# Performance work log

Measured on AMD Instinct MI355X. Metric: run time of the kernel, lower is better.

## Reference

```python
import jax, jax.numpy as jnp
import numpy as np

DIM = 1024
NUM_HEADS = 16
HEAD_DIM = DIM // NUM_HEADS
SCALE = HEAD_DIM ** -0.5
B, LQ, LK = 2, 2048, 2048


def setup_inputs() -> dict:
    key = jax.random.key(0)
    ks = jax.random.split(key, 12)
    init = 1.0 / np.sqrt(DIM)  # ~ torch Linear default scale
    inp = {
        "q": jax.random.normal(ks[0], (B, LQ, DIM), jnp.float32),
        "k": jax.random.normal(ks[1], (B, LK, DIM), jnp.float32),
        "v": jax.random.normal(ks[2], (B, LK, DIM), jnp.float32),
        "kv_mask": jnp.ones((B, LK), jnp.int32),
        "Wq": jax.random.uniform(ks[3], (DIM, DIM), jnp.float32, -init, init),
        "bq": jax.random.uniform(ks[4], (DIM,), jnp.float32, -init, init),
        "Wk": jax.random.uniform(ks[5], (DIM, DIM), jnp.float32, -init, init),
        "bk": jax.random.uniform(ks[6], (DIM,), jnp.float32, -init, init),
        "Wv": jax.random.uniform(ks[7], (DIM, DIM), jnp.float32, -init, init),
        "bv": jax.random.uniform(ks[8], (DIM,), jnp.float32, -init, init),
        "Wo": jax.random.uniform(ks[9], (DIM, DIM), jnp.float32, -init, init),
        "bo": jax.random.uniform(ks[10], (DIM,), jnp.float32, -init, init),
    }
    return inp


def reference(q, k, v, kv_mask, Wq, bq, Wk, bk, Wv, bv, Wo, bo):
    Bq, Lq, D = q.shape
    Lk = k.shape[1]
    H, Hd = NUM_HEADS, HEAD_DIM
    # projections (torch Linear: x @ W.T + b); split heads -> [B, H, L, Hd]
    qh = (q @ Wq.T + bq).reshape(Bq, Lq, H, Hd).transpose(0, 2, 1, 3)
    kh = (k @ Wk.T + bk).reshape(Bq, Lk, H, Hd).transpose(0, 2, 1, 3)
    vh = (v @ Wv.T + bv).reshape(Bq, Lk, H, Hd).transpose(0, 2, 1, 3)
    # scores [B, H, Lq, Lk]
    attn = jnp.einsum("bhqd,bhkd->bhqk", qh, kh) * SCALE
    mask = (kv_mask != 0)[:, None, None, :]
    attn = jnp.where(mask, attn, -jnp.inf)
    attn = jax.nn.softmax(attn, axis=-1)
    # dropout is identity at inference (p applied only in train mode)
    out = jnp.einsum("bhqk,bhkd->bhqd", attn, vh)
    out = out.transpose(0, 2, 1, 3).reshape(Bq, Lq, D)
    return out @ Wo.T + bo
```

## Files before the change

### kernel.cpp

```cpp
#include <hip/hip_runtime.h>
#include <stdint.h>

typedef unsigned short u16;
typedef __attribute__((ext_vector_type(8))) __bf16 bf16x8;
typedef __attribute__((ext_vector_type(4))) float f32x4;
typedef __attribute__((ext_vector_type(2))) unsigned int uint32x2;

#define DIM 1024
#define NH 16
#define HD 64
#define BSZ 2
#define LQ 2048
#define LK 2048
#define SCALE_LOG2E 0.18033688011112043f
#define MNEG -3.0e38f


static __device__ __forceinline__ float b2f(u16 u) {
  union { uint32_t i; float f; } v; v.i = ((uint32_t)u) << 16; return v.f;
}
static __device__ __forceinline__ u16 f2b(float f) {
  uint32_t x = __float_as_uint(f);
  return (u16)((x + 0x7fffu + ((x >> 16) & 1u)) >> 16);
}
static __device__ __forceinline__ uint32_t pk2r(float lo, float hi) {
  uint32_t a = __float_as_uint(lo) + 0x8000u;
  uint32_t b = __float_as_uint(hi) + 0x8000u;
  return __builtin_amdgcn_perm(b, a, 0x07060302u);
}
static __device__ __forceinline__ uint32_t cvtpk(float lo, float hi) {
  uint32_t r;
  asm("v_cvt_pk_bf16_f32 %0, %1, %2" : "=v"(r) : "v"(lo), "v"(hi));
  return r;
}
static __device__ __forceinline__ f32x4 zero4() {
  f32x4 z; z[0] = 0.f; z[1] = 0.f; z[2] = 0.f; z[3] = 0.f; return z;
}
static __device__ __forceinline__ float exp2c(float s) {
  float r;
  asm("v_exp_f32 %0, %1\n\ts_nop 0" : "=v"(r) : "v"(fminf(s, 30.0f)));
  return r;
}
static __device__ __forceinline__ void gload_lds16(const u16* g, u16* l) {
  __builtin_amdgcn_global_load_lds(
      (const __attribute__((address_space(1))) void*)g,
      (__attribute__((address_space(3))) void*)l, 16, 0, 0);
}

__global__ void mask_allvalid(const int* __restrict__ kvmask, int* allv) {
  int b = blockIdx.x;
  int base = b * LK + threadIdx.x * 8;
  int ok = 1;
#pragma unroll
  for (int j = 0; j < 8; ++j) ok &= (kvmask[base + j] != 0);
  unsigned long long m = __ballot(ok != 0);
  if ((threadIdx.x & 63) == 0 && m != ~0ULL) atomicAnd(&allv[b], 0);
}

struct ConvArgs {
  const float* src[11];
  long long cum[12];
  u16* dst;
};

__global__ void convert_inputs(ConvArgs ca) {
  long long c = (long long)blockIdx.x * blockDim.x + threadIdx.x;
  long long e0 = c * 8;
  if (e0 >= ca.cum[11]) return;
  int s = 0;
  while (e0 >= ca.cum[s + 1]) ++s;
  const float* sp = ca.src[s] + (e0 - ca.cum[s]);
  union { uint4 v; uint32_t w[4]; } t;
#pragma unroll
  for (int j = 0; j < 4; ++j) t.w[j] = pk2r(sp[2 * j], sp[2 * j + 1]);
  *(uint4*)(ca.dst + e0) = t.v;
}

struct GemmArgs {
  const u16* X[3];
  const u16* W[3];
  const u16* Bias[3];
  void* Y[3];
  float osc[3];
  int f32out;
  int vtz;
};

__global__ __launch_bounds__(256, 3) void gemm_bt_bias(GemmArgs ga) {
  const int K = DIM, N = DIM;
  __shared__ u16 smem[17408];
  u16* const Al = smem;
  u16* const Bl = smem + 8192;
  const int tid = threadIdx.x;
  const int wave = tid >> 6, lane = tid & 63;
  const int wm = wave >> 1, wn = wave & 1;
  const int lrow = lane & 15, quad = lane >> 4;
  const int z = blockIdx.z;
  const u16* X = ga.X[z];
  const u16* W = ga.W[z];
  const u16* Bias = ga.Bias[z];
  const float osc = ga.osc[z];
  const int m0 = blockIdx.x * 128;
  const int n0 = blockIdx.y * 128;

  f32x4 acc[4][4];
#pragma unroll
  for (int i = 0; i < 4; ++i)
#pragma unroll
    for (int j = 0; j < 4; ++j) acc[i][j] = zero4();

  const int cbase = wave * 256;
  for (int k0 = 0; k0 < K; k0 += 64) {
    __syncthreads();
#pragma unroll
    for (int i = 0; i < 4; ++i) {
      int c = cbase + i * 64 + lane;
      int row = c >> 3, colb = c & 7;
      gload_lds16(X + (size_t)(m0 + row) * K + k0 + colb * 8,
                  &Al[(cbase + i * 64) * 8]);
      gload_lds16(W + (size_t)(n0 + row) * K + k0 + colb * 8,
                  &Bl[(cbase + i * 64) * 8]);
    }
    __syncthreads();
#pragma unroll
    for (int ks = 0; ks < 2; ++ks) {
      bf16x8 af[4], bfr[4];
#pragma unroll
      for (int t = 0; t < 4; ++t)
        af[t] = *(const bf16x8*)&Al[(wm * 64 + t * 16 + lrow) * 64 + ks * 32 + quad * 8];
#pragma unroll
      for (int t = 0; t < 4; ++t)
        bfr[t] = *(const bf16x8*)&Bl[(wn * 64 + t * 16 + lrow) * 64 + ks * 32 + quad * 8];
#pragma unroll
      for (int mt = 0; mt < 4; ++mt)
#pragma unroll
        for (int nt = 0; nt < 4; ++nt)
          acc[mt][nt] = __builtin_amdgcn_mfma_f32_16x16x32_bf16(af[mt], bfr[nt], acc[mt][nt], 0, 0, 0);
    }
  }

  if (z == ga.vtz) {
    u16* Yv = (u16*)ga.Y[z];
    u16* const VT = smem;
    __syncthreads();
#pragma unroll
    for (int nt = 0; nt < 4; ++nt) {
      int colL = wn * 64 + nt * 16 + lrow;
      float bv = b2f(Bias[n0 + colL]);
#pragma unroll
      for (int mt = 0; mt < 4; ++mt) {
        int keyL = wm * 64 + mt * 16 + quad * 4;
        uint2 w;
        w.x = pk2r((acc[mt][nt][0] + bv) * osc, (acc[mt][nt][1] + bv) * osc);
        w.y = pk2r((acc[mt][nt][2] + bv) * osc, (acc[mt][nt][3] + bv) * osc);
        *(uint2*)&VT[colL * 136 + keyL] = w;
      }
    }
    __syncthreads();
    const int bb = m0 >> 11, key0 = m0 & 2047;
#pragma unroll
    for (int i = 0; i < 8; ++i) {
      int c = i * 256 + tid;
      int colL = c >> 4, k8 = c & 15;
      int hh = (n0 + colL) >> 6, dd = (n0 + colL) & 63;
      *(uint4*)(Yv + ((size_t)(bb * NH + hh) * HD + dd) * LK + key0 + k8 * 8) =
          *(const uint4*)&VT[colL * 136 + k8 * 8];
    }
  } else if (ga.f32out) {
    float* Yf = (float*)ga.Y[z];
#pragma unroll
    for (int nt = 0; nt < 4; ++nt) {
      int col = n0 + wn * 64 + nt * 16 + lrow;
      float bv = b2f(Bias[col]);
#pragma unroll
      for (int mt = 0; mt < 4; ++mt) {
        int rowb = m0 + wm * 64 + mt * 16 + quad * 4;
#pragma unroll
        for (int r = 0; r < 4; ++r)
          Yf[(size_t)(rowb + r) * N + col] = (acc[mt][nt][r] + bv) * osc;
      }
    }
  } else {
    u16* Yv = (u16*)ga.Y[z];
#pragma unroll
    for (int nt = 0; nt < 4; ++nt) {
      int col = n0 + wn * 64 + nt * 16 + lrow;
      float bv = b2f(Bias[col]);
#pragma unroll
      for (int mt = 0; mt < 4; ++mt) {
        int rowb = m0 + wm * 64 + mt * 16 + quad * 4;
#pragma unroll
        for (int r = 0; r < 4; ++r)
          Yv[(size_t)(rowb + r) * N + col] = f2b((acc[mt][nt][r] + bv) * osc);
      }
    }
  }
}

__global__ __launch_bounds__(256, 3) void attn_fused(
    const u16* __restrict__ qp, const u16* __restrict__ kp,
    const u16* __restrict__ vpt, const int* __restrict__ kvmask,
    const int* __restrict__ allv, u16* __restrict__ op,
    float* __restrict__ opart, float* __restrict__ lpart,
    int nsplit, int kspan) {
  __shared__ u16 Kl[128 * 64];
  __shared__ u16 Vt[64 * 128];
  __shared__ float Ml[128];
  const int tid = threadIdx.x;
  const int wave = tid >> 6, lane = tid & 63;
  const int lrow = lane & 15, quad = lane >> 4;
  const int bh = blockIdx.y;
  const int b = bh >> 4, h = bh & 15;
  const int q0 = blockIdx.x * 128;
  const int kc0 = blockIdx.z * kspan;
  const int kcend = kc0 + kspan;
  const bool av = (allv[b] != 0);

  const u16* qbase = qp + (size_t)b * LQ * DIM + h * HD;
  const u16* kbase = kp + (size_t)b * LK * DIM + h * HD;
  const u16* vtb = vpt + (size_t)(b * NH + h) * HD * LK;
  const int* mbase = kvmask + b * LK;
  const int wq0 = q0 + wave * 32;

  bf16x8 qf[2][2];
#pragma unroll
  for (int mt = 0; mt < 2; ++mt)
#pragma unroll
    for (int ks = 0; ks < 2; ++ks)
      qf[mt][ks] = *(const bf16x8*)(qbase + (size_t)(wq0 + mt * 16 + lrow) * DIM + ks * 32 + quad * 8);

  f32x4 acco[2][4];
  float lsum[2];
#pragma unroll
  for (int mt = 0; mt < 2; ++mt) {
#pragma unroll
    for (int dt = 0; dt < 4; ++dt) acco[mt][dt] = zero4();
    lsum[mt] = 0.0f;
  }

  const u16* kcur = kbase + (size_t)kc0 * DIM
      + (size_t)(wave * 8 + (lane >> 3)) * DIM + (((lane & 7) ^ (lane >> 3)) * 8);
  const u16* vcur = vtb + kc0
      + (size_t)(wave * 4 + (lane >> 4)) * LK
      + (((lane & 15) ^ ((4 * wave + (lane >> 4)) & 15)) * 8);
  u16* const Kldst = &Kl[wave * 512];
  u16* const Vtdst = &Vt[wave * 512];
  const int kread0 = lrow * 64 + ((quad ^ (lrow & 7)) * 8);
  const int kread1 = lrow * 64 + (((4 + quad) ^ (lrow & 7)) * 8);

  for (int kc = kc0; kc < kcend; kc += 128) {
    gload_lds16(kcur,                       Kldst);
    gload_lds16(kcur + (size_t)32 * DIM,    Kldst + 2048);
    gload_lds16(kcur + (size_t)64 * DIM,    Kldst + 4096);
    gload_lds16(kcur + (size_t)96 * DIM,    Kldst + 6144);
    gload_lds16(vcur,                       Vtdst);
    gload_lds16(vcur + (size_t)16 * LK,     Vtdst + 2048);
    gload_lds16(vcur + (size_t)32 * LK,     Vtdst + 4096);
    gload_lds16(vcur + (size_t)48 * LK,     Vtdst + 6144);
    if (!av && tid < 128) Ml[tid] = mbase[kc + tid] ? 0.0f : MNEG;
    __syncthreads();

#pragma unroll
    for (int kb = 0; kb < 4; ++kb) {
      f32x4 sacc[2][2];
#pragma unroll
      for (int mt = 0; mt < 2; ++mt)
#pragma unroll
        for (int ntl = 0; ntl < 2; ++ntl) sacc[mt][ntl] = zero4();
#pragma unroll
      for (int ks = 0; ks < 2; ++ks) {
#pragma unroll
        for (int ntl = 0; ntl < 2; ++ntl) {
          bf16x8 kf = *(const bf16x8*)&Kl[(2 * kb + ntl) * 1024 + (ks ? kread1 : kread0)];
          sacc[0][ntl] = __builtin_amdgcn_mfma_f32_16x16x32_bf16(kf, qf[0][ks], sacc[0][ntl], 0, 0, 0);
          sacc[1][ntl] = __builtin_amdgcn_mfma_f32_16x16x32_bf16(kf, qf[1][ks], sacc[1][ntl], 0, 0, 0);
        }
      }

      bf16x8 pf0, pf1;
#pragma unroll
      for (int mt = 0; mt < 2; ++mt) {
        float p0, p1, p2, p3, p4, p5, p6, p7;
        if (av) {
          p0 = exp2c(sacc[mt][0][0]); p1 = exp2c(sacc[mt][0][1]);
          p2 = exp2c(sacc[mt][0][2]); p3 = exp2c(sacc[mt][0][3]);
          p4 = exp2c(sacc[mt][1][0]); p5 = exp2c(sacc[mt][1][1]);
          p6 = exp2c(sacc[mt][1][2]); p7 = exp2c(sacc[mt][1][3]);
        } else {
          f32x4 mq0 = *(const f32x4*)&Ml[(2 * kb + 0) * 16 + quad * 4];
          f32x4 mq1 = *(const f32x4*)&Ml[(2 * kb + 1) * 16 + quad * 4];
          p0 = exp2c(sacc[mt][0][0] + mq0[0]); p1 = exp2c(sacc[mt][0][1] + mq0[1]);
          p2 = exp2c(sacc[mt][0][2] + mq0[2]); p3 = exp2c(sacc[mt][0][3] + mq0[3]);
          p4 = exp2c(sacc[mt][1][0] + mq1[0]); p5 = exp2c(sacc[mt][1][1] + mq1[1]);
          p6 = exp2c(sacc[mt][1][2] + mq1[2]); p7 = exp2c(sacc[mt][1][3] + mq1[3]);
        }
        lsum[mt] += ((p0 + p1) + (p2 + p3)) + ((p4 + p5) + (p6 + p7));
        uint32_t pw0 = cvtpk(p0, p1), pw1 = cvtpk(p2, p3);
        uint32_t pw2 = cvtpk(p4, p5), pw3 = cvtpk(p6, p7);
        uint32x2 sA = __builtin_amdgcn_permlane32_swap(pw0, pw2, false, false);
        uint32x2 sB = __builtin_amdgcn_permlane32_swap(pw1, pw3, false, false);
        uint32x2 tA = __builtin_amdgcn_permlane16_swap(sA.x, sA.y, false, false);
        uint32x2 tB = __builtin_amdgcn_permlane16_swap(sB.x, sB.y, false, false);
        union { uint32_t u[4]; bf16x8 v; } pu;
        pu.u[0] = tA.x; pu.u[1] = tB.x; pu.u[2] = tA.y; pu.u[3] = tB.y;
        if (mt == 0) pf0 = pu.v; else pf1 = pu.v;
      }

#pragma unroll
      for (int dt = 0; dt < 4; ++dt) {
        bf16x8 vf = *(const bf16x8*)&Vt[dt * 2048 + lrow * 128 + (((kb * 4 + quad) ^ lrow) * 8)];
        acco[0][dt] = __builtin_amdgcn_mfma_f32_16x16x32_bf16(vf, pf0, acco[0][dt], 0, 0, 0);
        acco[1][dt] = __builtin_amdgcn_mfma_f32_16x16x32_bf16(vf, pf1, acco[1][dt], 0, 0, 0);
      }
    }

    __syncthreads();
    kcur += (size_t)128 * DIM;
    vcur += 128;
  }

  if (nsplit > 1) {
    const int sidx = blockIdx.z;
    float* obs = opart + ((size_t)(sidx * BSZ + b) * LQ) * DIM + h * HD;
    float* lps = lpart + ((size_t)(sidx * BSZ + b) * NH + h) * LQ;
#pragma unroll
    for (int mt = 0; mt < 2; ++mt) {
      float t = lsum[mt];
      t += __shfl_xor(t, 16);
      t += __shfl_xor(t, 32);
      int q = wq0 + mt * 16 + lrow;
      if (quad == 0) lps[q] = t;
#pragma unroll
      for (int dt = 0; dt < 4; ++dt)
        *(f32x4*)&obs[(size_t)q * DIM + dt * 16 + quad * 4] = acco[mt][dt];
    }
  } else {
    u16* ob = op + (size_t)b * LQ * DIM + h * HD;
#pragma unroll
    for (int mt = 0; mt < 2; ++mt) {
      float t = lsum[mt];
      t += __shfl_xor(t, 16);
      t += __shfl_xor(t, 32);
      float inv = t > 0.0f ? 1.0f / t : 0.0f;
      int q = wq0 + mt * 16 + lrow;
#pragma unroll
      for (int dt = 0; dt < 4; ++dt) {
        uint2 w;
        w.x = pk2r(acco[mt][dt][0] * inv, acco[mt][dt][1] * inv);
        w.y = pk2r(acco[mt][dt][2] * inv, acco[mt][dt][3] * inv);
        *(uint2*)&ob[(size_t)q * DIM + dt * 16 + quad * 4] = w;
      }
    }
  }
}

__global__ void merge_splits(const float* __restrict__ opart,
                             const float* __restrict__ lpart,
                             u16* __restrict__ ao, int nsplit) {
  size_t e = ((size_t)blockIdx.x * blockDim.x + threadIdx.x) * 4;
  const size_t TOT = (size_t)BSZ * LQ * DIM;
  const size_t LSTRIDE = (size_t)BSZ * NH * LQ;
  if (e >= TOT) return;
  int col = (int)(e % DIM);
  int q = (int)((e / DIM) % LQ);
  int b = (int)(e / ((size_t)LQ * DIM));
  int h = col >> 6;
  size_t li = ((size_t)b * NH + h) * LQ + q;
  float l = 0.0f;
  f32x4 a = zero4();
  for (int s = 0; s < nsplit; ++s) {
    l += lpart[s * LSTRIDE + li];
    f32x4 c = *(const f32x4*)(opart + s * TOT + e);
    a[0] += c[0]; a[1] += c[1]; a[2] += c[2]; a[3] += c[3];
  }
  float inv = l > 0.0f ? 1.0f / l : 0.0f;
  uint2 w;
  w.x = pk2r(a[0] * inv, a[1] * inv);
  w.y = pk2r(a[2] * inv, a[3] * inv);
  *(uint2*)(ao + e) = w;
}

extern "C" void kernel_launch(void* const* d_in, const int* in_sizes, int n_in,
                              void* d_out, int out_size, void* d_ws, size_t ws_size,
                              hipStream_t stream) {
  (void)in_sizes; (void)n_in; (void)out_size;
  const int* kvmask = (const int*)d_in[3];

  u16* ws = (u16*)d_ws;
  const long long SQ = (long long)BSZ * LQ * DIM;
  const long long SW = (long long)DIM * DIM;
  const long long SB = DIM;
  long long cum[12];
  cum[0] = 0;
  cum[1] = cum[0] + SQ;
  cum[2] = cum[1] + SQ;
  cum[3] = cum[2] + SQ;
  cum[4] = cum[3] + SW;
  cum[5] = cum[4] + SW;
  cum[6] = cum[5] + SW;
  cum[7] = cum[6] + SW;
  cum[8] = cum[7] + SB;
  cum[9] = cum[8] + SB;
  cum[10] = cum[9] + SB;
  cum[11] = cum[10] + SB;
  const long long canon_end = cum[11];
  u16* cq  = ws + cum[0];
  u16* ck  = ws + cum[1];
  u16* cv  = ws + cum[2];
  u16* cWq = ws + cum[3];
  u16* cWk = ws + cum[4];
  u16* cWv = ws + cum[5];
  u16* cWo = ws + cum[6];
  u16* cbq = ws + cum[7];
  u16* cbk = ws + cum[8];
  u16* cbv = ws + cum[9];
  u16* cbo = ws + cum[10];
  u16* qp  = ws + canon_end;
  u16* kp  = qp + SQ;
  u16* vpt = kp + SQ;
  u16* ao  = vpt + SQ;
  int* allv = (int*)(ao + SQ);

  uintptr_t fbase = (((uintptr_t)(allv + 4)) + 15) & ~(uintptr_t)15;
  float* opart = (float*)fbase;
  const size_t TOT = (size_t)BSZ * LQ * DIM;
  const size_t LS  = (size_t)BSZ * NH * LQ;
  int nsplit = 1;
  {
    size_t base_off = fbase - (uintptr_t)d_ws;
    size_t need2 = base_off + 2 * (TOT + LS) * sizeof(float);
    if (ws_size >= need2) nsplit = 2;
  }
  float* lpart = opart + (size_t)nsplit * TOT;

  hipMemsetAsync(allv, 0xFF, 2 * sizeof(int), stream);
  mask_allvalid<<<BSZ, 256, 0, stream>>>(kvmask, allv);

  ConvArgs ca;
  ca.src[0] = (const float*)d_in[0];
  ca.src[1] = (const float*)d_in[1];
  ca.src[2] = (const float*)d_in[2];
  ca.src[3] = (const float*)d_in[4];
  ca.src[4] = (const float*)d_in[6];
  ca.src[5] = (const float*)d_in[8];
  ca.src[6] = (const float*)d_in[10];
  ca.src[7] = (const float*)d_in[5];
  ca.src[8] = (const float*)d_in[7];
  ca.src[9] = (const float*)d_in[9];
  ca.src[10] = (const float*)d_in[11];
  for (int i = 0; i < 12; ++i) ca.cum[i] = cum[i];
  ca.dst = ws;
  int conv_blocks = (int)((canon_end / 8 + 255) / 256);
  convert_inputs<<<conv_blocks, 256, 0, stream>>>(ca);

  const int M = BSZ * LQ;

  GemmArgs g1;
  g1.X[0] = cq; g1.W[0] = cWq; g1.Bias[0] = cbq; g1.Y[0] = qp;
  g1.X[1] = ck; g1.W[1] = cWk; g1.Bias[1] = cbk; g1.Y[1] = kp;
  g1.X[2] = cv; g1.W[2] = cWv; g1.Bias[2] = cbv; g1.Y[2] = vpt;
  g1.osc[0] = SCALE_LOG2E;
  g1.osc[1] = 1.0f;
  g1.osc[2] = 1.0f;
  g1.f32out = 0;
  g1.vtz = 2;
  gemm_bt_bias<<<dim3(M / 128, DIM / 128, 3), dim3(256), 0, stream>>>(g1);

  attn_fused<<<dim3(LQ / 128, BSZ * NH, nsplit), dim3(256), 0, stream>>>(
      qp, kp, vpt, kvmask, allv, ao, opart, lpart, nsplit, LK / nsplit);
  if (nsplit > 1) {
    int mblocks = (int)((TOT / 4 + 255) / 256);
    merge_splits<<<mblocks, 256, 0, stream>>>(opart, lpart, ao, nsplit);
  }

  GemmArgs g2;
  g2.X[0] = ao; g2.W[0] = cWo; g2.Bias[0] = cbo; g2.Y[0] = d_out;
  g2.X[1] = ao; g2.W[1] = cWo; g2.Bias[1] = cbo; g2.Y[1] = d_out;
  g2.X[2] = ao; g2.W[2] = cWo; g2.Bias[2] = cbo; g2.Y[2] = d_out;
  g2.osc[0] = 1.0f; g2.osc[1] = 1.0f; g2.osc[2] = 1.0f;
  g2.f32out = 1;
  g2.vtz = -1;
  gemm_bt_bias<<<dim3(M / 128, DIM / 128, 1), dim3(256), 0, stream>>>(g2);
}
```

Measured before the change: 243.3 us.

## Double-buffer K/V tiles in attention to overlap loads with MFMA compute

Allocates two LDS buffers for the K tile, the transposed V tile and the mask tile. The next chunk is prefetched into the alternate buffer right after the barrier, while the current chunk is consumed, which leaves one barrier per iteration instead of two. The aim is to hide global-to-LDS latency behind the QK/PV MFMA work. In exchange, LDS use per block roughly doubles and the launch-bounds occupancy hint drops from 3 to 2 blocks, so there is less latency hiding from co-resident blocks.

```diff
diff --git a/kernel.cpp b/kernel.cpp
--- a/kernel.cpp
+++ b/kernel.cpp
@@ -197,15 +197,15 @@
   }
 }
 
-__global__ __launch_bounds__(256, 3) void attn_fused(
+__global__ __launch_bounds__(256, 2) void attn_fused(
     const u16* __restrict__ qp, const u16* __restrict__ kp,
     const u16* __restrict__ vpt, const int* __restrict__ kvmask,
     const int* __restrict__ allv, u16* __restrict__ op,
     float* __restrict__ opart, float* __restrict__ lpart,
     int nsplit, int kspan) {
-  __shared__ u16 Kl[128 * 64];
-  __shared__ u16 Vt[64 * 128];
-  __shared__ float Ml[128];
+  __shared__ u16 Kl[2][128 * 64];
+  __shared__ u16 Vt[2][64 * 128];
+  __shared__ float Ml[2][128];
   const int tid = threadIdx.x;
   const int wave = tid >> 6, lane = tid & 63;
   const int lrow = lane & 15, quad = lane >> 4;
@@ -243,22 +243,47 @@
   const u16* vcur = vtb + kc0
       + (size_t)(wave * 4 + (lane >> 4)) * LK
       + (((lane & 15) ^ ((4 * wave + (lane >> 4)) & 15)) * 8);
-  u16* const Kldst = &Kl[wave * 512];
-  u16* const Vtdst = &Vt[wave * 512];
+  const int ldoff = wave * 512;
   const int kread0 = lrow * 64 + ((quad ^ (lrow & 7)) * 8);
   const int kread1 = lrow * 64 + (((4 + quad) ^ (lrow & 7)) * 8);
 
+  {
+    u16* Kd = &Kl[0][ldoff];
+    u16* Vd = &Vt[0][ldoff];
+    gload_lds16(kcur,                    Kd);
+    gload_lds16(kcur + (size_t)32 * DIM, Kd + 2048);
+    gload_lds16(kcur + (size_t)64 * DIM, Kd + 4096);
+    gload_lds16(kcur + (size_t)96 * DIM, Kd + 6144);
+    gload_lds16(vcur,                    Vd);
+    gload_lds16(vcur + (size_t)16 * LK,  Vd + 2048);
+    gload_lds16(vcur + (size_t)32 * LK,  Vd + 4096);
+    gload_lds16(vcur + (size_t)48 * LK,  Vd + 6144);
+    if (!av && tid < 128) Ml[0][tid] = mbase[kc0 + tid] ? 0.0f : MNEG;
+  }
+
+  int buf = 0;
   for (int kc = kc0; kc < kcend; kc += 128) {
-    gload_lds16(kcur,                       Kldst);
-    gload_lds16(kcur + (size_t)32 * DIM,    Kldst + 2048);
-    gload_lds16(kcur + (size_t)64 * DIM,    Kldst + 4096);
-    gload_lds16(kcur + (size_t)96 * DIM,    Kldst + 6144);
-    gload_lds16(vcur,                       Vtdst);
-    gload_lds16(vcur + (size_t)16 * LK,     Vtdst + 2048);
-    gload_lds16(vcur + (size_t)32 * LK,     Vtdst + 4096);
-    gload_lds16(vcur + (size_t)48 * LK,     Vtdst + 6144);
-    if (!av && tid < 128) Ml[tid] = mbase[kc + tid] ? 0.0f : MNEG;
     __syncthreads();
+
+    if (kc + 128 < kcend) {
+      const u16* kn = kcur + (size_t)128 * DIM;
+      const u16* vn = vcur + 128;
+      u16* Kd = &Kl[buf ^ 1][ldoff];
+      u16* Vd = &Vt[buf ^ 1][ldoff];
+      gload_lds16(kn,                    Kd);
+      gload_lds16(kn + (size_t)32 * DIM, Kd + 2048);
+      gload_lds16(kn + (size_t)64 * DIM, Kd + 4096);
+      gload_lds16(kn + (size_t)96 * DIM, Kd + 6144);
+      gload_lds16(vn,                    Vd);
+      gload_lds16(vn + (size_t)16 * LK,  Vd + 2048);
+      gload_lds16(vn + (size_t)32 * LK,  Vd + 4096);
+      gload_lds16(vn + (size_t)48 * LK,  Vd + 6144);
+      if (!av && tid < 128) Ml[buf ^ 1][tid] = mbase[kc + 128 + tid] ? 0.0f : MNEG;
+    }
+
+    const u16* Klb = Kl[buf];
+    const u16* Vtb = Vt[buf];
+    const float* Mlb = Ml[buf];
 
 #pragma unroll
     for (int kb = 0; kb < 4; ++kb) {
@@ -271,7 +296,7 @@
       for (int ks = 0; ks < 2; ++ks) {
 #pragma unroll
         for (int ntl = 0; ntl < 2; ++ntl) {
-          bf16x8 kf = *(const bf16x8*)&Kl[(2 * kb + ntl) * 1024 + (ks ? kread1 : kread0)];
+          bf16x8 kf = *(const bf16x8*)&Klb[(2 * kb + ntl) * 1024 + (ks ? kread1 : kread0)];
           sacc[0][ntl] = __builtin_amdgcn_mfma_f32_16x16x32_bf16(kf, qf[0][ks], sacc[0][ntl], 0, 0, 0);
           sacc[1][ntl] = __builtin_amdgcn_mfma_f32_16x16x32_bf16(kf, qf[1][ks], sacc[1][ntl], 0, 0, 0);
         }
@@ -287,8 +312,8 @@
           p4 = exp2c(sacc[mt][1][0]); p5 = exp2c(sacc[mt][1][1]);
           p6 = exp2c(sacc[mt][1][2]); p7 = exp2c(sacc[mt][1][3]);
         } else {
-          f32x4 mq0 = *(const f32x4*)&Ml[(2 * kb + 0) * 16 + quad * 4];
-          f32x4 mq1 = *(const f32x4*)&Ml[(2 * kb + 1) * 16 + quad * 4];
+          f32x4 mq0 = *(const f32x4*)&Mlb[(2 * kb + 0) * 16 + quad * 4];
+          f32x4 mq1 = *(const f32x4*)&Mlb[(2 * kb + 1) * 16 + quad * 4];
           p0 = exp2c(sacc[mt][0][0] + mq0[0]); p1 = exp2c(sacc[mt][0][1] + mq0[1]);
           p2 = exp2c(sacc[mt][0][2] + mq0[2]); p3 = exp2c(sacc[mt][0][3] + mq0[3]);
           p4 = exp2c(sacc[mt][1][0] + mq1[0]); p5 = exp2c(sacc[mt][1][1] + mq1[1]);
@@ -308,13 +333,13 @@
 
 #pragma unroll
       for (int dt = 0; dt < 4; ++dt) {
-        bf16x8 vf = *(const bf16x8*)&Vt[dt * 2048 + lrow * 128 + (((kb * 4 + quad) ^ lrow) * 8)];
+        bf16x8 vf = *(const bf16x8*)&Vtb[dt * 2048 + lrow * 128 + (((kb * 4 + quad) ^ lrow) * 8)];
         acco[0][dt] = __builtin_amdgcn_mfma_f32_16x16x32_bf16(vf, pf0, acco[0][dt], 0, 0, 0);
         acco[1][dt] = __builtin_amdgcn_mfma_f32_16x16x32_bf16(vf, pf1, acco[1][dt], 0, 0, 0);
       }
     }
 
-    __syncthreads();
+    buf ^= 1;
     kcur += (size_t)128 * DIM;
     vcur += 128;
   }
```

Result: slower. 251.5 us (+3.3%).
